# Kernel tuning notes

Measured on AMD Instinct MI355X. Metric: run time of the kernel, lower is better.

The kernel has to match this reference:

```python
import jax, jax.numpy as jnp
import numpy as np

B, S, H = 4, 2048, 2048
E, K = 4, 2
FF = 4 * H  # standard MLP expert expansion


def setup_inputs() -> dict:
    key = jax.random.key(0)
    ks = jax.random.split(key, 5)
    sc = 0.02
    return {
        "hidden_states": jax.random.normal(ks[0], (B, S, H), jnp.float32),
        "w_gate": jax.random.normal(ks[1], (H, E), jnp.float32) * sc,
        "b_gate": jnp.zeros((E,), jnp.float32),
        "w1": jax.random.normal(ks[2], (E, H, FF), jnp.float32) * sc,
        "b1": jnp.zeros((E, FF), jnp.float32),
        "w2": jax.random.normal(ks[3], (E, FF, H), jnp.float32) * sc,
        "b2": jnp.zeros((E, H), jnp.float32),
    }


def reference(hidden_states, w_gate, b_gate, w1, b1, w2, b2):
    # Router: linear gate -> softmax -> top-k, renormalized gate weights
    logits = jnp.einsum("bsh,he->bse", hidden_states, w_gate) + b_gate
    probs = jax.nn.softmax(logits, axis=-1)                       # [B,S,E]
    top_p, top_i = jax.lax.top_k(probs, K)                        # [B,S,K]
    gate_w = top_p / jnp.sum(top_p, axis=-1, keepdims=True)

    # Switch-style load-balancing aux loss
    route = jax.nn.one_hot(top_i, E, dtype=probs.dtype)           # [B,S,K,E]
    frac_tokens = jnp.mean(jnp.sum(route, axis=2) / K, axis=(0, 1))  # [E]
    mean_prob = jnp.mean(probs, axis=(0, 1))                      # [E]
    aux_loss = E * jnp.sum(frac_tokens * mean_prob)

    # Dispatch/combine: small fixed expert count -> loop over experts,
    # dense FFN on all tokens, mask via gate weight (0 for unrouted tokens).
    out = jnp.zeros_like(hidden_states)
    for e in range(E):
        w_e = jnp.sum(gate_w * (top_i == e), axis=-1)             # [B,S]
        h = jax.nn.gelu(jnp.einsum("bsh,hf->bsf", hidden_states, w1[e]) + b1[e])
        y = jnp.einsum("bsf,fh->bsh", h, w2[e]) + b2[e]
        out = out + w_e[..., None] * y
    return out, aux_loss
```

## Files before the change

kernel.cpp:

```cpp
#include <hip/hip_runtime.h>

typedef unsigned short u16;
typedef __attribute__((ext_vector_type(8))) short bf16x8;
typedef __attribute__((ext_vector_type(4))) float f32x4;

#define TOK  8192
#define HD   2048
#define FFD  8192
#define NEXP 4
#define CAPE 4352

#define S_BARRIER() asm volatile("s_barrier" ::: "memory")
#define VMCNT(n)    asm volatile("s_waitcnt vmcnt(" #n ")" ::: "memory")

__device__ __forceinline__ u16 f2bf(float f){
  unsigned u = __float_as_uint(f);
  u += 0x7fffu + ((u >> 16) & 1u);
  return (u16)(u >> 16);
}

__device__ __forceinline__ float gelu_tanh(float x){
  float u = 0.7978845608028654f * (x + 0.044715f * x * x * x);
  return 0.5f * x * (1.0f + tanhf(u));
}

__device__ __forceinline__ void gload_lds16(const void* g, void* l){
  __builtin_amdgcn_global_load_lds((const __attribute__((address_space(1))) void*)g,
                                   (__attribute__((address_space(3))) void*)l, 16, 0, 0);
}

__device__ __forceinline__ f32x4 mfma_bf16(bf16x8 a, bf16x8 b, f32x4 c){
  asm("v_mfma_f32_16x16x32_bf16 %0, %1, %2, %0" : "+v"(c) : "v"(a), "v"(b));
  return c;
}

__global__ __launch_bounds__(256) void cvt_to_bf16(const float* __restrict__ in,
                                                   u16* __restrict__ out, int n4){
  int i = blockIdx.x * 256 + threadIdx.x;
  if (i >= n4) return;
  float4 v = ((const float4*)in)[i];
  ushort4 o;
  o.x = f2bf(v.x); o.y = f2bf(v.y); o.z = f2bf(v.z); o.w = f2bf(v.w);
  ((ushort4*)out)[i] = o;
}

__global__ __launch_bounds__(256) void transpose_cvt(const float* __restrict__ in,
                                                     u16* __restrict__ out, int R, int C){
  __shared__ float tile[64][65];
  int tx = threadIdx.x & 63;
  int ty = threadIdx.x >> 6;
  size_t r0 = (size_t)blockIdx.y * 64;
  size_t c0 = (size_t)blockIdx.x * 64;
  #pragma unroll
  for (int i = ty; i < 64; i += 4)
    tile[i][tx] = in[(r0 + i) * C + (c0 + tx)];
  __syncthreads();
  #pragma unroll
  for (int i = ty; i < 64; i += 4)
    out[(c0 + i) * R + (r0 + tx)] = f2bf(tile[tx][i]);
}

__global__ __launch_bounds__(256) void router_kernel(
    const float* __restrict__ X, const float* __restrict__ wg, const float* __restrict__ bg,
    float* __restrict__ probs, int* __restrict__ topi, float* __restrict__ gatew){
  int t = blockIdx.x;
  const float* x = X + (size_t)t * HD;
  float a0 = 0.f, a1 = 0.f, a2 = 0.f, a3 = 0.f;
  for (int h = threadIdx.x; h < HD; h += 256){
    float xv = x[h];
    float4 w = ((const float4*)wg)[h];
    a0 += xv * w.x; a1 += xv * w.y; a2 += xv * w.z; a3 += xv * w.w;
  }
  __shared__ float red[4][256];
  red[0][threadIdx.x] = a0; red[1][threadIdx.x] = a1;
  red[2][threadIdx.x] = a2; red[3][threadIdx.x] = a3;
  __syncthreads();
  for (int s = 128; s > 0; s >>= 1){
    if (threadIdx.x < (unsigned)s){
      #pragma unroll
      for (int e = 0; e < 4; e++) red[e][threadIdx.x] += red[e][threadIdx.x + s];
    }
    __syncthreads();
  }
  if (threadIdx.x == 0){
    float l[4], p[4];
    #pragma unroll
    for (int e = 0; e < 4; e++) l[e] = red[e][0] + bg[e];
    float mx = fmaxf(fmaxf(l[0], l[1]), fmaxf(l[2], l[3]));
    float s = 0.f;
    #pragma unroll
    for (int e = 0; e < 4; e++){ p[e] = expf(l[e] - mx); s += p[e]; }
    #pragma unroll
    for (int e = 0; e < 4; e++){ p[e] /= s; probs[t * 4 + e] = p[e]; }
    int e0 = 0;
    for (int e = 1; e < 4; e++) if (p[e] > p[e0]) e0 = e;
    int e1 = -1;
    for (int e = 0; e < 4; e++){ if (e == e0) continue; if (e1 < 0 || p[e] > p[e1]) e1 = e; }
    float g = p[e0] + p[e1];
    topi[t * 2] = e0; topi[t * 2 + 1] = e1;
    #pragma unroll
    for (int e = 0; e < 4; e++)
      gatew[(size_t)e * TOK + t] = (e == e0) ? p[e0] / g : (e == e1) ? p[e1] / g : 0.f;
  }
}

__global__ __launch_bounds__(256) void build_lists(const int* __restrict__ topi,
                                                   int* __restrict__ cnt,
                                                   int* __restrict__ lists){
  int t = blockIdx.x * 256 + threadIdx.x;
  if (t >= TOK) return;
  #pragma unroll
  for (int k = 0; k < 2; k++){
    int e = topi[t * 2 + k];
    int p = atomicAdd(cnt + e, 1);
    lists[e * TOK + p] = t;
  }
}

__global__ __launch_bounds__(256) void aux_kernel(const float* __restrict__ probs,
                                                  const int* __restrict__ topi,
                                                  float* __restrict__ out_aux){
  __shared__ float sp[4][256];
  __shared__ float sc[4][256];
  float p[4] = {0,0,0,0}, c[4] = {0,0,0,0};
  for (int t = threadIdx.x; t < TOK; t += 256){
    #pragma unroll
    for (int e = 0; e < 4; e++) p[e] += probs[t * 4 + e];
    c[topi[t * 2]]     += 1.f;
    c[topi[t * 2 + 1]] += 1.f;
  }
  #pragma unroll
  for (int e = 0; e < 4; e++){ sp[e][threadIdx.x] = p[e]; sc[e][threadIdx.x] = c[e]; }
  __syncthreads();
  for (int s = 128; s > 0; s >>= 1){
    if (threadIdx.x < (unsigned)s){
      #pragma unroll
      for (int e = 0; e < 4; e++){
        sp[e][threadIdx.x] += sp[e][threadIdx.x + s];
        sc[e][threadIdx.x] += sc[e][threadIdx.x + s];
      }
    }
    __syncthreads();
  }
  if (threadIdx.x == 0){
    float aux = 0.f;
    #pragma unroll
    for (int e = 0; e < 4; e++)
      aux += (sc[e][0] / (float)(TOK * 2)) * (sp[e][0] / (float)TOK);
    *out_aux = 4.f * aux;
  }
}

__global__ __launch_bounds__(512, 2) void gemm1_8p(
    const u16* __restrict__ Xb, const u16* __restrict__ BT,
    const int* __restrict__ rowidx, const int* __restrict__ cntp,
    const float* __restrict__ bias, u16* __restrict__ Hout)
{
  __shared__ __align__(16) u16 As[2 * 256 * 64];
  __shared__ __align__(16) u16 Bs[2 * 256 * 64];
  const int Mv = *cntp;
  const int nwg = gridDim.x * gridDim.y;
  const int orig = blockIdx.x + gridDim.x * blockIdx.y;
  const int q8 = nwg >> 3, r8 = nwg & 7, xcd = orig & 7, rank = orig >> 3;
  const int v = (xcd < r8 ? xcd * (q8 + 1) : r8 * (q8 + 1) + (xcd - r8) * q8) + rank;
  const int by = v % (int)gridDim.y, bx = v / (int)gridDim.y;
  const int browg = by * 256;
  if (browg >= Mv) return;
  const size_t bcol = (size_t)bx * 256;

  const int tid = threadIdx.x, lane = tid & 63, w = tid >> 6;
  const int wr = w >> 2, wc = w & 3;
  const int l8 = lane >> 3;
  const int csw  = ((lane & 7) ^ l8) * 8;
  const int sw   = (lane & 7) * 8;
  const int h8   = ((lane >> 4) & 3) * 8;
  const int colk0 = h8 ^ sw, colk1 = (32 | h8) ^ sw;
  const int r16 = lane & 15;

  const u16* bsrc[4]; int bch[4];
  #pragma unroll
  for (int j = 0; j < 4; j++){
    int rb = wc * 64 + wr * 32 + j * 8;
    bch[j] = rb * 128;
    bsrc[j] = BT + (bcol + rb + l8) * (size_t)HD + csw;
  }
  const u16* asrc[4]; int ach[4];
  #pragma unroll
  for (int q = 0; q < 4; q++){
    int rb = wr * 128 + q * 32 + wc * 8;
    ach[q] = rb * 128;
    int rl = browg + rb + l8; if (rl > Mv - 1) rl = Mv - 1;
    asrc[q] = Xb + (size_t)rowidx[rl] * HD + csw;
  }

  f32x4 acc[8][4];
  #pragma unroll
  for (int m = 0; m < 8; m++)
    #pragma unroll
    for (int n = 0; n < 4; n++) acc[m][n] = (f32x4){0.f, 0.f, 0.f, 0.f};
  bf16x8 bC[8];

  const int NT = HD / 64;
  #pragma unroll
  for (int j = 0; j < 4; j++) gload_lds16(bsrc[j], (char*)Bs + bch[j]);
  #pragma unroll
  for (int q = 0; q < 4; q++) gload_lds16(asrc[q], (char*)As + ach[q]);
  VMCNT(3); S_BARRIER();

  for (int t = 0; t < NT; ++t){
    const u16* asb = As + (t & 1) * 16384;
    const u16* bsb = Bs + (t & 1) * 16384;
    char* anb = (char*)As + ((t & 1) ^ 1) * 32768;
    char* bnb = (char*)Bs + ((t & 1) ^ 1) * 32768;
    const size_t ko = (size_t)(t + 1) * 64;
    const bool lastT = (t == NT - 1);
    #pragma unroll 4
    for (int p = 0; p < 4; p++){
      if (p == 0){
        #pragma unroll
        for (int nf = 0; nf < 4; nf++){
          const u16* bp = bsb + (wc * 64 + nf * 16 + r16) * 64;
          bC[nf * 2]     = *(const bf16x8*)(bp + colk0);
          bC[nf * 2 + 1] = *(const bf16x8*)(bp + colk1);
        }
      }
      bf16x8 a[2][2];
      #pragma unroll
      for (int mi = 0; mi < 2; mi++){
        const u16* ap = asb + (wr * 128 + (2 * p + mi) * 16 + r16) * 64;
        a[mi][0] = *(const bf16x8*)(ap + colk0);
        a[mi][1] = *(const bf16x8*)(ap + colk1);
      }
      if (!lastT){
        if      (p == 0){ gload_lds16(bsrc[0] + ko, bnb + bch[0]); gload_lds16(bsrc[1] + ko, bnb + bch[1]); }
        else if (p == 1){ gload_lds16(bsrc[2] + ko, bnb + bch[2]); gload_lds16(bsrc[3] + ko, bnb + bch[3]); }
        else if (p == 2){ gload_lds16(asrc[0] + ko, anb + ach[0]); gload_lds16(asrc[1] + ko, anb + ach[1]); }
        else            { gload_lds16(asrc[2] + ko, anb + ach[2]); gload_lds16(asrc[3] + ko, anb + ach[3]); }
      }
      S_BARRIER();
      __builtin_amdgcn_s_setprio(1);
      #pragma unroll
      for (int mi = 0; mi < 2; mi++)
        #pragma unroll
        for (int nf = 0; nf < 4; nf++){
          acc[2 * p + mi][nf] = mfma_bf16(a[mi][0], bC[nf * 2],     acc[2 * p + mi][nf]);
          acc[2 * p + mi][nf] = mfma_bf16(a[mi][1], bC[nf * 2 + 1], acc[2 * p + mi][nf]);
        }
      __builtin_amdgcn_s_setprio(0);
      if (!lastT){ if (p == 0) VMCNT(4); else if (p == 1) VMCNT(5); else if (p == 2) VMCNT(6); else VMCNT(3); }
      else       { if (p == 0) VMCNT(2); else if (p == 1) VMCNT(1); else if (p == 2) VMCNT(0); }
      S_BARRIER();
    }
  }

  const int cl = r16, rg = (lane >> 4) * 4;
  const size_t c0 = bcol + wc * 64;
  float bv[4];
  #pragma unroll
  for (int nf = 0; nf < 4; nf++) bv[nf] = bias[c0 + nf * 16 + cl];
  #pragma unroll
  for (int mf = 0; mf < 8; mf++){
    const size_t rb = (size_t)(browg + wr * 128 + mf * 16 + rg);
    #pragma unroll
    for (int nf = 0; nf < 4; nf++){
      const size_t col = c0 + nf * 16 + cl;
      #pragma unroll
      for (int j = 0; j < 4; j++)
        Hout[(rb + j) * FFD + col] = f2bf(gelu_tanh(acc[mf][nf][j] + bv[nf]));
    }
  }
}

__global__ __launch_bounds__(256) void gemm2_97(
    const u16* __restrict__ Hb, const u16* __restrict__ BT,
    const int* __restrict__ rowidx, const int* __restrict__ cntp,
    const float* __restrict__ bias, const float* __restrict__ gate,
    float* __restrict__ Cout)
{
  __shared__ __align__(16) u16 As[128 * 64];
  __shared__ __align__(16) u16 Bs[128 * 64];
  const int Mv = *cntp;
  const int nwg = gridDim.x * gridDim.y;
  const int orig = blockIdx.x + gridDim.x * blockIdx.y;
  const int q8 = nwg >> 3, r8 = nwg & 7, xcd = orig & 7, rank = orig >> 3;
  const int v = (xcd < r8 ? xcd * (q8 + 1) : r8 * (q8 + 1) + (xcd - r8) * q8) + rank;
  const int bx = v % (int)gridDim.x, by = v / (int)gridDim.x;
  const int browg = by * 128;
  if (browg >= Mv) return;
  const size_t bcol = (size_t)bx * 128;

  const int tid = threadIdx.x, lane = tid & 63, w = tid >> 6;
  const int wr = w >> 1, wc = w & 1;
  const int l8 = lane >> 3;
  const int csw  = ((lane & 7) ^ l8) * 8;
  const int sw   = (lane & 7) * 8;
  const int h8   = ((lane >> 4) & 3) * 8;
  const int colk0 = h8 ^ sw, colk1 = (32 | h8) ^ sw;
  const int r16 = lane & 15;

  const u16* bsrc[4]; int bch[4];
  #pragma unroll
  for (int j = 0; j < 4; j++){
    int rb = j * 32 + w * 8;
    bch[j] = rb * 128;
    bsrc[j] = BT + (bcol + rb + l8) * (size_t)FFD + csw;
  }
  const u16* asrc[4]; int ach[4];
  #pragma unroll
  for (int q = 0; q < 4; q++){
    int rb = wr * 64 + q * 16 + wc * 8;
    ach[q] = rb * 128;
    asrc[q] = Hb + (size_t)(browg + rb + l8) * FFD + csw;
  }

  f32x4 acc[4][4];
  #pragma unroll
  for (int m = 0; m < 4; m++)
    #pragma unroll
    for (int n = 0; n < 4; n++) acc[m][n] = (f32x4){0.f, 0.f, 0.f, 0.f};
  bf16x8 bC[8];

  const int NT = FFD / 64;
  for (int t = 0; t < NT; ++t){
    const size_t ko = (size_t)t * 64;
    __syncthreads();
    #pragma unroll
    for (int j = 0; j < 4; j++) gload_lds16(bsrc[j] + ko, (char*)Bs + bch[j]);
    #pragma unroll
    for (int q = 0; q < 4; q++) gload_lds16(asrc[q] + ko, (char*)As + ach[q]);
    __syncthreads();

    #pragma unroll
    for (int nf = 0; nf < 4; nf++){
      const u16* bp = Bs + (wc * 64 + nf * 16 + r16) * 64;
      bC[nf * 2]     = *(const bf16x8*)(bp + colk0);
      bC[nf * 2 + 1] = *(const bf16x8*)(bp + colk1);
    }
    #pragma unroll
    for (int m = 0; m < 4; m++){
      const u16* ap = As + (wr * 64 + m * 16 + r16) * 64;
      bf16x8 a0 = *(const bf16x8*)(ap + colk0);
      bf16x8 a1 = *(const bf16x8*)(ap + colk1);
      #pragma unroll
      for (int nf = 0; nf < 4; nf++){
        acc[m][nf] = mfma_bf16(a0, bC[nf * 2],     acc[m][nf]);
        acc[m][nf] = mfma_bf16(a1, bC[nf * 2 + 1], acc[m][nf]);
      }
    }
  }

  const int cl = r16, rg = (lane >> 4) * 4;
  const size_t c0 = bcol + wc * 64;
  float bv[4];
  #pragma unroll
  for (int nf = 0; nf < 4; nf++) bv[nf] = bias[c0 + nf * 16 + cl];
  #pragma unroll
  for (int mf = 0; mf < 4; mf++){
    const int rbase = browg + wr * 64 + mf * 16 + rg;
    int   tok[4]; float gv[4];
    #pragma unroll
    for (int j = 0; j < 4; j++){
      const bool ok = (rbase + j) < Mv;
      tok[j] = ok ? rowidx[rbase + j] : -1;
      gv[j]  = ok ? gate[tok[j]] : 0.f;
    }
    #pragma unroll
    for (int nf = 0; nf < 4; nf++){
      const size_t col = c0 + nf * 16 + cl;
      #pragma unroll
      for (int j = 0; j < 4; j++){
        if (tok[j] >= 0){
          const size_t idx = (size_t)tok[j] * HD + col;
          Cout[idx] += gv[j] * (acc[mf][nf][j] + bv[nf]);
        }
      }
    }
  }
}

extern "C" void kernel_launch(void* const* d_in, const int* in_sizes, int n_in,
                              void* d_out, int out_size, void* d_ws, size_t ws_size,
                              hipStream_t stream){
  (void)in_sizes; (void)n_in; (void)ws_size;
  const float* X  = (const float*)d_in[0];
  const float* wg = (const float*)d_in[1];
  const float* bg = (const float*)d_in[2];
  const float* w1 = (const float*)d_in[3];
  const float* b1 = (const float*)d_in[4];
  const float* w2 = (const float*)d_in[5];
  const float* b2 = (const float*)d_in[6];
  float* out = (float*)d_out;

  char* ws = (char*)d_ws;
  size_t off = 0;
  auto alloc = [&](size_t b) -> char* {
    char* p = ws + off;
    off = (off + b + 255) & ~(size_t)255;
    return p;
  };
  u16*   Xb    = (u16*)  alloc((size_t)TOK * HD * 2);
  u16*   W1T   = (u16*)  alloc((size_t)FFD * HD * 2);
  u16*   W2T   = (u16*)  alloc((size_t)HD * FFD * 2);
  float* probs = (float*)alloc((size_t)TOK * 4 * 4);
  int*   topi  = (int*)  alloc((size_t)TOK * 2 * 4);
  float* gatew = (float*)alloc((size_t)NEXP * TOK * 4);
  int*   cnt   = (int*)  alloc((size_t)NEXP * 4);
  int*   lists = (int*)  alloc((size_t)NEXP * TOK * 4);
  u16*   Hb    = (u16*)  alloc((size_t)CAPE * FFD * 2);

  hipMemsetAsync(cnt, 0, NEXP * sizeof(int), stream);
  hipMemsetAsync(out, 0, (size_t)TOK * HD * sizeof(float), stream);

  cvt_to_bf16<<<(TOK * HD / 4 + 255) / 256, 256, 0, stream>>>(X, Xb, TOK * HD / 4);
  router_kernel<<<TOK, 256, 0, stream>>>(X, wg, bg, probs, topi, gatew);
  build_lists<<<TOK / 256, 256, 0, stream>>>(topi, cnt, lists);
  aux_kernel<<<1, 256, 0, stream>>>(probs, topi, out + (out_size - 1));

  for (int e = 0; e < NEXP; ++e){
    transpose_cvt<<<dim3(FFD / 64, HD / 64), 256, 0, stream>>>(
        w1 + (size_t)e * HD * FFD, W1T, HD, FFD);
    transpose_cvt<<<dim3(HD / 64, FFD / 64), 256, 0, stream>>>(
        w2 + (size_t)e * FFD * HD, W2T, FFD, HD);
    gemm1_8p<<<dim3(FFD / 256, CAPE / 256), 512, 0, stream>>>(
        Xb, W1T, lists + e * TOK, cnt + e, b1 + (size_t)e * FFD, Hb);
    gemm2_97<<<dim3(HD / 128, CAPE / 128), 256, 0, stream>>>(
        Hb, W2T, lists + e * TOK, cnt + e, b2 + (size_t)e * HD,
        gatew + (size_t)e * TOK, out);
  }
}
```

Measured before the change: 1.837 ms.

## Rework weight transpose tiles, gemm1 load schedule, and XCD tile mapping

The weight transpose-convert kernel now converts to bf16 before staging in LDS, uses 128x64 tiles and writes packed ushort2 outputs, which cuts shared-memory traffic and makes the global stores wider. The gemm1 main loop is unrolled by hand into four phases, with reordered async global-to-LDS loads and simpler vmcnt waits. Both GEMMs get a new XCD-aware block mapping that gives each XCD a contiguous band of column tiles, with the intent of improving L2 reuse of the weights. The new mapping assumes gridDim.x is divisible by 8, and the changed wait counts could introduce load/compute hazards.

After: 1.775 ms. -3.4%, faster.

```diff
diff --git a/kernel.cpp b/kernel.cpp
--- a/kernel.cpp
+++ b/kernel.cpp
@@ -46,18 +46,25 @@
 
 __global__ __launch_bounds__(256) void transpose_cvt(const float* __restrict__ in,
                                                      u16* __restrict__ out, int R, int C){
-  __shared__ float tile[64][65];
-  int tx = threadIdx.x & 63;
-  int ty = threadIdx.x >> 6;
-  size_t r0 = (size_t)blockIdx.y * 64;
-  size_t c0 = (size_t)blockIdx.x * 64;
-  #pragma unroll
-  for (int i = ty; i < 64; i += 4)
-    tile[i][tx] = in[(r0 + i) * C + (c0 + tx)];
+  __shared__ u16 t[64][138];
+  const int tx = threadIdx.x & 63;
+  const int w  = threadIdx.x >> 6;
+  const size_t r0 = (size_t)blockIdx.y * 128;
+  const size_t c0 = (size_t)blockIdx.x * 64;
+  #pragma unroll
+  for (int i = 0; i < 32; i++){
+    const int r = w * 32 + i;
+    t[tx][r] = f2bf(in[(r0 + r) * C + c0 + tx]);
+  }
   __syncthreads();
   #pragma unroll
-  for (int i = ty; i < 64; i += 4)
-    out[(c0 + i) * R + (r0 + tx)] = f2bf(tile[tx][i]);
+  for (int j = 0; j < 16; j++){
+    const int c = j * 4 + w;
+    ushort2 o;
+    o.x = t[c][2 * tx];
+    o.y = t[c][2 * tx + 1];
+    *(ushort2*)(out + (c0 + c) * (size_t)R + r0 + 2 * tx) = o;
+  }
 }
 
 __global__ __launch_bounds__(256) void router_kernel(
@@ -159,38 +166,34 @@
   __shared__ __align__(16) u16 As[2 * 256 * 64];
   __shared__ __align__(16) u16 Bs[2 * 256 * 64];
   const int Mv = *cntp;
-  const int nwg = gridDim.x * gridDim.y;
-  const int orig = blockIdx.x + gridDim.x * blockIdx.y;
-  const int q8 = nwg >> 3, r8 = nwg & 7, xcd = orig & 7, rank = orig >> 3;
-  const int v = (xcd < r8 ? xcd * (q8 + 1) : r8 * (q8 + 1) + (xcd - r8) * q8) + rank;
-  const int by = v % (int)gridDim.y, bx = v / (int)gridDim.y;
+  const int gx = gridDim.x, gy = gridDim.y;
+  const int orig = blockIdx.x + gx * blockIdx.y;
+  const int xcd = orig & 7, rank = orig >> 3;
+  const int bxl = rank / gy, by = rank % gy;
+  const int bx = xcd * (gx >> 3) + bxl;
   const int browg = by * 256;
   if (browg >= Mv) return;
   const size_t bcol = (size_t)bx * 256;
 
   const int tid = threadIdx.x, lane = tid & 63, w = tid >> 6;
-  const int wr = w >> 2, wc = w & 3;
+  const int wm = w >> 2, wn = w & 3;
   const int l8 = lane >> 3;
-  const int csw  = ((lane & 7) ^ l8) * 8;
-  const int sw   = (lane & 7) * 8;
-  const int h8   = ((lane >> 4) & 3) * 8;
-  const int colk0 = h8 ^ sw, colk1 = (32 | h8) ^ sw;
+  const int csw = ((lane & 7) ^ l8) * 8;
+  const int sw  = (lane & 7) * 8;
+  const int h8  = ((lane >> 4) & 3) * 8;
+  const int colk0 = h8 ^ sw, colk1 = (32 + h8) ^ sw;
   const int r16 = lane & 15;
 
   const u16* bsrc[4]; int bch[4];
-  #pragma unroll
-  for (int j = 0; j < 4; j++){
-    int rb = wc * 64 + wr * 32 + j * 8;
-    bch[j] = rb * 128;
-    bsrc[j] = BT + (bcol + rb + l8) * (size_t)HD + csw;
-  }
   const u16* asrc[4]; int ach[4];
   #pragma unroll
-  for (int q = 0; q < 4; q++){
-    int rb = wr * 128 + q * 32 + wc * 8;
-    ach[q] = rb * 128;
+  for (int i = 0; i < 4; i++){
+    const int rb = i * 64 + w * 8;
+    bch[i] = rb * 128;
+    ach[i] = rb * 128;
+    bsrc[i] = BT + (bcol + rb + l8) * (size_t)HD + csw;
     int rl = browg + rb + l8; if (rl > Mv - 1) rl = Mv - 1;
-    asrc[q] = Xb + (size_t)rowidx[rl] * HD + csw;
+    asrc[i] = Xb + (size_t)rowidx[rl] * HD + csw;
   }
 
   f32x4 acc[8][4];
@@ -201,66 +204,127 @@
   bf16x8 bC[8];
 
   const int NT = HD / 64;
-  #pragma unroll
-  for (int j = 0; j < 4; j++) gload_lds16(bsrc[j], (char*)Bs + bch[j]);
-  #pragma unroll
-  for (int q = 0; q < 4; q++) gload_lds16(asrc[q], (char*)As + ach[q]);
-  VMCNT(3); S_BARRIER();
+
+  gload_lds16(bsrc[0], (char*)Bs + bch[0]);
+  gload_lds16(bsrc[1], (char*)Bs + bch[1]);
+  gload_lds16(bsrc[2], (char*)Bs + bch[2]);
+  gload_lds16(bsrc[3], (char*)Bs + bch[3]);
+  gload_lds16(asrc[0], (char*)As + ach[0]);
+  gload_lds16(asrc[2], (char*)As + ach[2]);
+  gload_lds16(asrc[1], (char*)As + ach[1]);
+  gload_lds16(asrc[3], (char*)As + ach[3]);
+  VMCNT(2); S_BARRIER();
 
   for (int t = 0; t < NT; ++t){
-    const u16* asb = As + (t & 1) * 16384;
-    const u16* bsb = Bs + (t & 1) * 16384;
-    char* anb = (char*)As + ((t & 1) ^ 1) * 32768;
-    char* bnb = (char*)Bs + ((t & 1) ^ 1) * 32768;
+    const u16* Ac = As + (t & 1) * 16384;
+    const u16* Bc = Bs + (t & 1) * 16384;
+    char* An = (char*)As + ((t & 1) ^ 1) * 32768;
+    char* Bn = (char*)Bs + ((t & 1) ^ 1) * 32768;
     const size_t ko = (size_t)(t + 1) * 64;
-    const bool lastT = (t == NT - 1);
-    #pragma unroll 4
-    for (int p = 0; p < 4; p++){
-      if (p == 0){
-        #pragma unroll
-        for (int nf = 0; nf < 4; nf++){
-          const u16* bp = bsb + (wc * 64 + nf * 16 + r16) * 64;
-          bC[nf * 2]     = *(const bf16x8*)(bp + colk0);
-          bC[nf * 2 + 1] = *(const bf16x8*)(bp + colk1);
-        }
+    const bool more = (t < NT - 1);
+
+    {
+      #pragma unroll
+      for (int nf = 0; nf < 4; nf++){
+        const u16* bp = Bc + (wn * 64 + nf * 16 + r16) * 64;
+        bC[nf * 2]     = *(const bf16x8*)(bp + colk0);
+        bC[nf * 2 + 1] = *(const bf16x8*)(bp + colk1);
       }
       bf16x8 a[2][2];
       #pragma unroll
       for (int mi = 0; mi < 2; mi++){
-        const u16* ap = asb + (wr * 128 + (2 * p + mi) * 16 + r16) * 64;
+        const u16* ap = Ac + (wm * 128 + mi * 16 + r16) * 64;
         a[mi][0] = *(const bf16x8*)(ap + colk0);
         a[mi][1] = *(const bf16x8*)(ap + colk1);
       }
-      if (!lastT){
-        if      (p == 0){ gload_lds16(bsrc[0] + ko, bnb + bch[0]); gload_lds16(bsrc[1] + ko, bnb + bch[1]); }
-        else if (p == 1){ gload_lds16(bsrc[2] + ko, bnb + bch[2]); gload_lds16(bsrc[3] + ko, bnb + bch[3]); }
-        else if (p == 2){ gload_lds16(asrc[0] + ko, anb + ach[0]); gload_lds16(asrc[1] + ko, anb + ach[1]); }
-        else            { gload_lds16(asrc[2] + ko, anb + ach[2]); gload_lds16(asrc[3] + ko, anb + ach[3]); }
-      }
+      if (more){ gload_lds16(bsrc[0] + ko, Bn + bch[0]); gload_lds16(bsrc[1] + ko, Bn + bch[1]); }
       S_BARRIER();
       __builtin_amdgcn_s_setprio(1);
       #pragma unroll
       for (int mi = 0; mi < 2; mi++)
         #pragma unroll
         for (int nf = 0; nf < 4; nf++){
-          acc[2 * p + mi][nf] = mfma_bf16(a[mi][0], bC[nf * 2],     acc[2 * p + mi][nf]);
-          acc[2 * p + mi][nf] = mfma_bf16(a[mi][1], bC[nf * 2 + 1], acc[2 * p + mi][nf]);
+          acc[mi][nf] = mfma_bf16(a[mi][0], bC[nf * 2],     acc[mi][nf]);
+          acc[mi][nf] = mfma_bf16(a[mi][1], bC[nf * 2 + 1], acc[mi][nf]);
         }
       __builtin_amdgcn_s_setprio(0);
-      if (!lastT){ if (p == 0) VMCNT(4); else if (p == 1) VMCNT(5); else if (p == 2) VMCNT(6); else VMCNT(3); }
-      else       { if (p == 0) VMCNT(2); else if (p == 1) VMCNT(1); else if (p == 2) VMCNT(0); }
+      S_BARRIER();
+    }
+    {
+      bf16x8 a[2][2];
+      #pragma unroll
+      for (int mi = 0; mi < 2; mi++){
+        const u16* ap = Ac + (wm * 128 + (2 + mi) * 16 + r16) * 64;
+        a[mi][0] = *(const bf16x8*)(ap + colk0);
+        a[mi][1] = *(const bf16x8*)(ap + colk1);
+      }
+      if (more){ gload_lds16(bsrc[2] + ko, Bn + bch[2]); gload_lds16(bsrc[3] + ko, Bn + bch[3]); }
+      S_BARRIER();
+      __builtin_amdgcn_s_setprio(1);
+      #pragma unroll
+      for (int mi = 0; mi < 2; mi++)
+        #pragma unroll
+        for (int nf = 0; nf < 4; nf++){
+          acc[2 + mi][nf] = mfma_bf16(a[mi][0], bC[nf * 2],     acc[2 + mi][nf]);
+          acc[2 + mi][nf] = mfma_bf16(a[mi][1], bC[nf * 2 + 1], acc[2 + mi][nf]);
+        }
+      __builtin_amdgcn_s_setprio(0);
+      VMCNT(4);
+      S_BARRIER();
+    }
+    {
+      bf16x8 a[2][2];
+      #pragma unroll
+      for (int mi = 0; mi < 2; mi++){
+        const u16* ap = Ac + (wm * 128 + (4 + mi) * 16 + r16) * 64;
+        a[mi][0] = *(const bf16x8*)(ap + colk0);
+        a[mi][1] = *(const bf16x8*)(ap + colk1);
+      }
+      if (more){ gload_lds16(asrc[0] + ko, An + ach[0]); gload_lds16(asrc[2] + ko, An + ach[2]); }
+      S_BARRIER();
+      __builtin_amdgcn_s_setprio(1);
+      #pragma unroll
+      for (int mi = 0; mi < 2; mi++)
+        #pragma unroll
+        for (int nf = 0; nf < 4; nf++){
+          acc[4 + mi][nf] = mfma_bf16(a[mi][0], bC[nf * 2],     acc[4 + mi][nf]);
+          acc[4 + mi][nf] = mfma_bf16(a[mi][1], bC[nf * 2 + 1], acc[4 + mi][nf]);
+        }
+      __builtin_amdgcn_s_setprio(0);
+      S_BARRIER();
+    }
+    {
+      bf16x8 a[2][2];
+      #pragma unroll
+      for (int mi = 0; mi < 2; mi++){
+        const u16* ap = Ac + (wm * 128 + (6 + mi) * 16 + r16) * 64;
+        a[mi][0] = *(const bf16x8*)(ap + colk0);
+        a[mi][1] = *(const bf16x8*)(ap + colk1);
+      }
+      if (more){ gload_lds16(asrc[1] + ko, An + ach[1]); gload_lds16(asrc[3] + ko, An + ach[3]); }
+      S_BARRIER();
+      __builtin_amdgcn_s_setprio(1);
+      #pragma unroll
+      for (int mi = 0; mi < 2; mi++)
+        #pragma unroll
+        for (int nf = 0; nf < 4; nf++){
+          acc[6 + mi][nf] = mfma_bf16(a[mi][0], bC[nf * 2],     acc[6 + mi][nf]);
+          acc[6 + mi][nf] = mfma_bf16(a[mi][1], bC[nf * 2 + 1], acc[6 + mi][nf]);
+        }
+      __builtin_amdgcn_s_setprio(0);
+      if (more){ if (t == NT - 2) VMCNT(0); else VMCNT(2); }
       S_BARRIER();
     }
   }
 
   const int cl = r16, rg = (lane >> 4) * 4;
-  const size_t c0 = bcol + wc * 64;
+  const size_t c0 = bcol + wn * 64;
   float bv[4];
   #pragma unroll
   for (int nf = 0; nf < 4; nf++) bv[nf] = bias[c0 + nf * 16 + cl];
   #pragma unroll
   for (int mf = 0; mf < 8; mf++){
-    const size_t rb = (size_t)(browg + wr * 128 + mf * 16 + rg);
+    const size_t rb = (size_t)(browg + wm * 128 + mf * 16 + rg);
     #pragma unroll
     for (int nf = 0; nf < 4; nf++){
       const size_t col = c0 + nf * 16 + cl;
@@ -280,11 +344,11 @@
   __shared__ __align__(16) u16 As[128 * 64];
   __shared__ __align__(16) u16 Bs[128 * 64];
   const int Mv = *cntp;
-  const int nwg = gridDim.x * gridDim.y;
-  const int orig = blockIdx.x + gridDim.x * blockIdx.y;
-  const int q8 = nwg >> 3, r8 = nwg & 7, xcd = orig & 7, rank = orig >> 3;
-  const int v = (xcd < r8 ? xcd * (q8 + 1) : r8 * (q8 + 1) + (xcd - r8) * q8) + rank;
-  const int bx = v % (int)gridDim.x, by = v / (int)gridDim.x;
+  const int gx = gridDim.x, gy = gridDim.y;
+  const int orig = blockIdx.x + gx * blockIdx.y;
+  const int xcd = orig & 7, rank = orig >> 3;
+  const int bxl = rank / gy, by = rank % gy;
+  const int bx = xcd * (gx >> 3) + bxl;
   const int browg = by * 128;
   if (browg >= Mv) return;
   const size_t bcol = (size_t)bx * 128;
@@ -295,7 +359,7 @@
   const int csw  = ((lane & 7) ^ l8) * 8;
   const int sw   = (lane & 7) * 8;
   const int h8   = ((lane >> 4) & 3) * 8;
-  const int colk0 = h8 ^ sw, colk1 = (32 | h8) ^ sw;
+  const int colk0 = h8 ^ sw, colk1 = (32 + h8) ^ sw;
   const int r16 = lane & 15;
 
   const u16* bsrc[4]; int bch[4];
@@ -417,9 +481,9 @@
   aux_kernel<<<1, 256, 0, stream>>>(probs, topi, out + (out_size - 1));
 
   for (int e = 0; e < NEXP; ++e){
-    transpose_cvt<<<dim3(FFD / 64, HD / 64), 256, 0, stream>>>(
+    transpose_cvt<<<dim3(FFD / 64, HD / 128), 256, 0, stream>>>(
         w1 + (size_t)e * HD * FFD, W1T, HD, FFD);
-    transpose_cvt<<<dim3(HD / 64, FFD / 64), 256, 0, stream>>>(
+    transpose_cvt<<<dim3(HD / 64, FFD / 128), 256, 0, stream>>>(
         w2 + (size_t)e * FFD * HD, W2T, FFD, HD);
     gemm1_8p<<<dim3(FFD / 256, CAPE / 256), 512, 0, stream>>>(
         Xb, W1T, lists + e * TOK, cnt + e, b1 + (size_t)e * FFD, Hb);
```
